# Performance work log

Measured on AMD Instinct MI355X. Metric: run time of the kernel, lower is better.

The kernel has to match this reference:

```python
import jax, jax.numpy as jnp
import numpy as np

SIZE, DIM, BATCH, K = 131072, 128, 1024, 16


def _l2_normalize(x, axis):
    return x / jnp.linalg.norm(x, axis=axis, keepdims=True)


def setup_inputs() -> dict:
    key = jax.random.key(0)
    k1, k2, k3, k4, k5 = jax.random.split(key, 5)
    # bank init as in MemoryBank._create: uniform in [-std, std], then l2-normalized rows
    std = 1.0 / np.sqrt(DIM / 3)
    bank = jax.random.uniform(k1, (SIZE, DIM), dtype=jnp.float32) * (2 * std) - std
    bank = _l2_normalize(bank, 1)
    emb_batch = _l2_normalize(jax.random.normal(k2, (BATCH, DIM), dtype=jnp.float32), 1)
    data_memory = _l2_normalize(jax.random.normal(k3, (BATCH, DIM), dtype=jnp.float32), 1)
    idxs = jax.random.randint(k4, (BATCH, K), 0, SIZE)
    update_indices = jax.random.randint(k5, (BATCH,), 0, SIZE)
    return {
        "emb_batch": emb_batch,
        "data_memory": data_memory,
        "bank": bank,
        "idxs": idxs,
        "update_indices": update_indices,
    }


def reference(emb_batch, data_memory, bank, idxs, update_indices):
    # get_all_dot_products: [B, S]
    all_dots = jnp.matmul(emb_batch, bank.T)
    # get_all_distances: ||b_j - e_i||. Original materializes [B,S,D] differences;
    # mathematically identical expansion avoids the huge intermediate.
    e_sq = jnp.sum(emb_batch * emb_batch, axis=1)[:, None]   # [B,1]
    b_sq = jnp.sum(bank * bank, axis=1)[None, :]             # [1,S]
    distances = jnp.sqrt(jnp.maximum(e_sq + b_sq - 2.0 * all_dots, 0.0))  # [B,S]
    # get_dot_products with 2D idxs: gather [B,K,D] then multiply-sum -> [B,K]
    knn_dots = jnp.einsum("bkd,bd->bk", bank[idxs], emb_batch)
    # update: scatter rows of data_memory into the bank
    new_bank = bank.at[update_indices].set(data_memory)
    return distances, all_dots, knn_dots, new_bank
```

## Files before the change

### kernel.cpp

```cpp
#include <hip/hip_runtime.h>
#include <hip/hip_bf16.h>

typedef __bf16 bf16x8 __attribute__((ext_vector_type(8)));
typedef float  f32x4  __attribute__((ext_vector_type(4)));

#define SIZE_  131072
#define DIM_   128
#define BATCH_ 1024
#define KNN_   16

#define BM 256
#define BN 64

__global__ __launch_bounds__(256) void prep_emb(const float* __restrict__ emb,
                                                __bf16* __restrict__ emb16,
                                                float* __restrict__ e_sq) {
    int wid  = (blockIdx.x * 256 + threadIdx.x) >> 6;
    int lane = threadIdx.x & 63;
    float2 v = *reinterpret_cast<const float2*>(emb + (size_t)wid * DIM_ + lane * 2);
    float s = v.x * v.x + v.y * v.y;
    #pragma unroll
    for (int off = 32; off; off >>= 1) s += __shfl_xor(s, off);
    union { __bf16 h[2]; unsigned int u; } pk;
    pk.h[0] = (__bf16)v.x; pk.h[1] = (__bf16)v.y;
    *reinterpret_cast<unsigned int*>(emb16 + (size_t)wid * DIM_ + lane * 2) = pk.u;
    if (lane == 0) e_sq[wid] = s;
}

__global__ __launch_bounds__(256) void prep_bank(const float* __restrict__ bank,
                                                 float* __restrict__ newbank,
                                                 float* __restrict__ b_sq) {
    int wid  = (blockIdx.x * 256 + threadIdx.x) >> 6;
    int lane = threadIdx.x & 63;
    size_t base = (size_t)wid * DIM_ + lane * 2;
    float2 v = *reinterpret_cast<const float2*>(bank + base);
    *reinterpret_cast<float2*>(newbank + base) = v;
    float s = v.x * v.x + v.y * v.y;
    #pragma unroll
    for (int off = 32; off; off >>= 1) s += __shfl_xor(s, off);
    if (lane == 0) b_sq[wid] = s;
}

__global__ __launch_bounds__(256) void gemm_dist(const float* __restrict__ bank,
                                                 const __bf16* __restrict__ emb16,
                                                 const float* __restrict__ e_sq,
                                                 const float* __restrict__ b_sq,
                                                 float* __restrict__ out_dist,
                                                 float* __restrict__ out_dots) {
    __shared__ __bf16 lA[BM * DIM_];
    __shared__ __bf16 lB[BN * DIM_];
    char* lAc = (char*)lA;
    char* lBc = (char*)lB;

    int bid = blockIdx.x;
    int logical = (bid & 7) * (8192 / 8) + (bid >> 3);
    int mt = logical & 3;
    int nt = logical >> 2;
    int m0 = mt * BM;
    int n0 = nt * BN;
    int tid = threadIdx.x;

    {
        const char* src = (const char*)(emb16 + (size_t)m0 * DIM_);
        #pragma unroll
        for (int i = 0; i < 16; ++i) {
            int o   = (i * 256 + tid) * 16;
            int row = o >> 8;
            int so  = o ^ ((row & 7) << 4);
            *reinterpret_cast<int4*>(lAc + so) = *reinterpret_cast<const int4*>(src + o);
        }
    }
    {
        #pragma unroll
        for (int i = 0; i < 4; ++i) {
            int p   = i * 256 + tid;
            int row = p >> 4;
            int k0  = (p & 15) * 8;
            const f32x4* s4 = reinterpret_cast<const f32x4*>(bank + (size_t)(n0 + row) * DIM_ + k0);
            f32x4 a = s4[0], b = s4[1];
            union { __bf16 h[8]; int4 v; } pk;
            pk.h[0] = (__bf16)a.x; pk.h[1] = (__bf16)a.y; pk.h[2] = (__bf16)a.z; pk.h[3] = (__bf16)a.w;
            pk.h[4] = (__bf16)b.x; pk.h[5] = (__bf16)b.y; pk.h[6] = (__bf16)b.z; pk.h[7] = (__bf16)b.w;
            int o  = (row << 8) + k0 * 2;
            int so = o ^ ((row & 7) << 4);
            *reinterpret_cast<int4*>(lBc + so) = pk.v;
        }
    }
    __syncthreads();

    int wv   = tid >> 6;
    int lane = tid & 63;
    int lr   = lane & 15;
    int lkb  = (lane >> 4) * 8;
    int rgrp = lane >> 4;

    f32x4 acc[4][4] = {};

    #pragma unroll
    for (int ks = 0; ks < 4; ++ks) {
        int kk = ks * 32 + lkb;
        bf16x8 af[4], bf[4];
        #pragma unroll
        for (int mr = 0; mr < 4; ++mr) {
            int row = wv * 64 + mr * 16 + lr;
            int o   = (row << 8) + kk * 2;
            af[mr]  = *reinterpret_cast<const bf16x8*>(lAc + (o ^ ((row & 7) << 4)));
        }
        #pragma unroll
        for (int nc = 0; nc < 4; ++nc) {
            int row = nc * 16 + lr;
            int o   = (row << 8) + kk * 2;
            bf[nc]  = *reinterpret_cast<const bf16x8*>(lBc + (o ^ ((row & 7) << 4)));
        }
        #pragma unroll
        for (int mr = 0; mr < 4; ++mr)
            #pragma unroll
            for (int nc = 0; nc < 4; ++nc)
                acc[mr][nc] = __builtin_amdgcn_mfma_f32_16x16x32_bf16(af[mr], bf[nc], acc[mr][nc], 0, 0, 0);
    }

    float bs[4];
    #pragma unroll
    for (int nc = 0; nc < 4; ++nc) bs[nc] = b_sq[n0 + nc * 16 + lr];
    float es[4][4];
    #pragma unroll
    for (int mr = 0; mr < 4; ++mr)
        #pragma unroll
        for (int j = 0; j < 4; ++j)
            es[mr][j] = e_sq[m0 + wv * 64 + mr * 16 + rgrp * 4 + j];

    __syncthreads();
    char* ftile = lAc;

    #pragma unroll
    for (int pass = 0; pass < 2; ++pass) {
        #pragma unroll
        for (int mr = 0; mr < 4; ++mr) {
            #pragma unroll
            for (int j = 0; j < 4; ++j) {
                int row = wv * 64 + mr * 16 + rgrp * 4 + j;
                #pragma unroll
                for (int nc = 0; nc < 4; ++nc) {
                    float d = acc[mr][nc][j];
                    float val;
                    if (pass == 0) {
                        float arg = es[mr][j] + bs[nc] - 2.0f * d;
                        val = sqrtf(fmaxf(arg, 0.0f));
                    } else {
                        val = d;
                    }
                    int o = (row << 8) + (nc * 16 + lr) * 4;
                    *reinterpret_cast<float*>(ftile + (o ^ ((row & 7) << 4))) = val;
                }
            }
        }
        __syncthreads();
        float* outp = pass ? out_dots : out_dist;
        int g  = tid >> 4;
        int c4 = tid & 15;
        #pragma unroll
        for (int i = 0; i < 16; ++i) {
            int row = i * 16 + g;
            int o   = (row << 8) + c4 * 16;
            f32x4 v = *reinterpret_cast<const f32x4*>(ftile + (o ^ ((row & 7) << 4)));
            size_t ga = (size_t)(m0 + row) * SIZE_ + n0 + c4 * 4;
            __builtin_nontemporal_store(v, reinterpret_cast<f32x4*>(outp + ga));
        }
        __syncthreads();
    }
}

__global__ __launch_bounds__(128) void scatter_rows(const float* __restrict__ dmem,
                                                    const int* __restrict__ upd,
                                                    float* __restrict__ newbank) {
    int i = blockIdx.x;
    int idx = upd[i];
    __shared__ int dup;
    if (threadIdx.x == 0) dup = 0;
    __syncthreads();
    for (int j = i + 1 + threadIdx.x; j < BATCH_; j += 128)
        if (upd[j] == idx) dup = 1;
    __syncthreads();
    if (dup) return;
    newbank[(size_t)idx * DIM_ + threadIdx.x] = dmem[(size_t)i * DIM_ + threadIdx.x];
}

__global__ __launch_bounds__(256) void knn_kernel(const float* __restrict__ bank,
                                                  const float* __restrict__ emb,
                                                  const int* __restrict__ idxs,
                                                  float* __restrict__ knn) {
    int wid  = (blockIdx.x * 256 + threadIdx.x) >> 6;
    int lane = threadIdx.x & 63;
    int b    = wid >> 4;
    int idx  = idxs[wid];
    float2 br = *reinterpret_cast<const float2*>(bank + (size_t)idx * DIM_ + lane * 2);
    float2 er = *reinterpret_cast<const float2*>(emb + (size_t)b * DIM_ + lane * 2);
    float s = br.x * er.x + br.y * er.y;
    #pragma unroll
    for (int off = 32; off; off >>= 1) s += __shfl_xor(s, off);
    if (lane == 0) knn[wid] = s;
}

extern "C" void kernel_launch(void* const* d_in, const int* in_sizes, int n_in,
                              void* d_out, int out_size, void* d_ws, size_t ws_size,
                              hipStream_t stream) {
    const float* emb  = (const float*)d_in[0];
    const float* dmem = (const float*)d_in[1];
    const float* bank = (const float*)d_in[2];
    const int*   idxs = (const int*)d_in[3];
    const int*   upd  = (const int*)d_in[4];

    float* out       = (float*)d_out;
    float* out_dist  = out;
    float* out_dots  = out + (size_t)BATCH_ * SIZE_;
    float* out_knn   = out + (size_t)2 * BATCH_ * SIZE_;
    float* out_bank  = out_knn + (size_t)BATCH_ * KNN_;

    char*   ws    = (char*)d_ws;
    float*  b_sq  = (float*)ws;
    float*  e_sq  = (float*)(ws + 524288);
    __bf16* emb16 = (__bf16*)(ws + 528384);

    prep_emb <<<BATCH_ / 4,      256, 0, stream>>>(emb, emb16, e_sq);
    prep_bank<<<SIZE_ / 4,       256, 0, stream>>>(bank, out_bank, b_sq);
    gemm_dist<<<(BATCH_ / BM) * (SIZE_ / BN), 256, 0, stream>>>(bank, emb16, e_sq, b_sq, out_dist, out_dots);
    scatter_rows<<<BATCH_,       128, 0, stream>>>(dmem, upd, out_bank);
    knn_kernel<<<(BATCH_ * KNN_) / 4, 256, 0, stream>>>(bank, emb, idxs, out_knn);
}
```

Before: 274.8 us.

## Fuse bank copy and squared-norm into GEMM kernel, halve M tile

Removes the separate prep_bank kernel. The GEMM blocks now compute each bank row's squared norm from the fp32 tile they already load, keep it in shared memory, and have the mt==0 blocks write the bank copy with nontemporal stores. BM drops from 256 to 128, which doubles the grid and makes each bank tile get loaded and converted 8 times instead of 4. In exchange for that extra bank read traffic, it saves one kernel launch, a full pass over the bank, and the b_sq buffer round trip.

```diff
diff --git a/kernel.cpp b/kernel.cpp
--- a/kernel.cpp
+++ b/kernel.cpp
@@ -9,8 +9,10 @@
 #define BATCH_ 1024
 #define KNN_   16
 
-#define BM 256
+#define BM 128
 #define BN 64
+#define MT (BATCH_ / BM)
+#define NT (SIZE_ / BN)
 
 __global__ __launch_bounds__(256) void prep_emb(const float* __restrict__ emb,
                                                 __bf16* __restrict__ emb16,
@@ -27,35 +29,22 @@
     if (lane == 0) e_sq[wid] = s;
 }
 
-__global__ __launch_bounds__(256) void prep_bank(const float* __restrict__ bank,
-                                                 float* __restrict__ newbank,
-                                                 float* __restrict__ b_sq) {
-    int wid  = (blockIdx.x * 256 + threadIdx.x) >> 6;
-    int lane = threadIdx.x & 63;
-    size_t base = (size_t)wid * DIM_ + lane * 2;
-    float2 v = *reinterpret_cast<const float2*>(bank + base);
-    *reinterpret_cast<float2*>(newbank + base) = v;
-    float s = v.x * v.x + v.y * v.y;
-    #pragma unroll
-    for (int off = 32; off; off >>= 1) s += __shfl_xor(s, off);
-    if (lane == 0) b_sq[wid] = s;
-}
-
 __global__ __launch_bounds__(256) void gemm_dist(const float* __restrict__ bank,
                                                  const __bf16* __restrict__ emb16,
                                                  const float* __restrict__ e_sq,
-                                                 const float* __restrict__ b_sq,
                                                  float* __restrict__ out_dist,
-                                                 float* __restrict__ out_dots) {
+                                                 float* __restrict__ out_dots,
+                                                 float* __restrict__ out_bank) {
     __shared__ __bf16 lA[BM * DIM_];
     __shared__ __bf16 lB[BN * DIM_];
+    __shared__ float  bsq[BN];
     char* lAc = (char*)lA;
     char* lBc = (char*)lB;
 
     int bid = blockIdx.x;
-    int logical = (bid & 7) * (8192 / 8) + (bid >> 3);
-    int mt = logical & 3;
-    int nt = logical >> 2;
+    int logical = (bid & 7) * (16384 / 8) + (bid >> 3);
+    int mt = logical & (MT - 1);
+    int nt = logical >> 3;
     int m0 = mt * BM;
     int n0 = nt * BN;
     int tid = threadIdx.x;
@@ -63,7 +52,7 @@
     {
         const char* src = (const char*)(emb16 + (size_t)m0 * DIM_);
         #pragma unroll
-        for (int i = 0; i < 16; ++i) {
+        for (int i = 0; i < 8; ++i) {
             int o   = (i * 256 + tid) * 16;
             int row = o >> 8;
             int so  = o ^ ((row & 7) << 4);
@@ -76,8 +65,18 @@
             int p   = i * 256 + tid;
             int row = p >> 4;
             int k0  = (p & 15) * 8;
-            const f32x4* s4 = reinterpret_cast<const f32x4*>(bank + (size_t)(n0 + row) * DIM_ + k0);
+            size_t gb = (size_t)(n0 + row) * DIM_ + k0;
+            const f32x4* s4 = reinterpret_cast<const f32x4*>(bank + gb);
             f32x4 a = s4[0], b = s4[1];
+            if (mt == 0) {
+                __builtin_nontemporal_store(a, reinterpret_cast<f32x4*>(out_bank + gb));
+                __builtin_nontemporal_store(b, reinterpret_cast<f32x4*>(out_bank + gb + 4));
+            }
+            float s = a.x * a.x + a.y * a.y + a.z * a.z + a.w * a.w
+                    + b.x * b.x + b.y * b.y + b.z * b.z + b.w * b.w;
+            #pragma unroll
+            for (int off = 8; off; off >>= 1) s += __shfl_xor(s, off);
+            if ((p & 15) == 0) bsq[row] = s;
             union { __bf16 h[8]; int4 v; } pk;
             pk.h[0] = (__bf16)a.x; pk.h[1] = (__bf16)a.y; pk.h[2] = (__bf16)a.z; pk.h[3] = (__bf16)a.w;
             pk.h[4] = (__bf16)b.x; pk.h[5] = (__bf16)b.y; pk.h[6] = (__bf16)b.z; pk.h[7] = (__bf16)b.w;
@@ -94,15 +93,15 @@
     int lkb  = (lane >> 4) * 8;
     int rgrp = lane >> 4;
 
-    f32x4 acc[4][4] = {};
+    f32x4 acc[2][4] = {};
 
     #pragma unroll
     for (int ks = 0; ks < 4; ++ks) {
         int kk = ks * 32 + lkb;
-        bf16x8 af[4], bf[4];
-        #pragma unroll
-        for (int mr = 0; mr < 4; ++mr) {
-            int row = wv * 64 + mr * 16 + lr;
+        bf16x8 af[2], bf[4];
+        #pragma unroll
+        for (int mr = 0; mr < 2; ++mr) {
+            int row = wv * 32 + mr * 16 + lr;
             int o   = (row << 8) + kk * 2;
             af[mr]  = *reinterpret_cast<const bf16x8*>(lAc + (o ^ ((row & 7) << 4)));
         }
@@ -113,7 +112,7 @@
             bf[nc]  = *reinterpret_cast<const bf16x8*>(lBc + (o ^ ((row & 7) << 4)));
         }
         #pragma unroll
-        for (int mr = 0; mr < 4; ++mr)
+        for (int mr = 0; mr < 2; ++mr)
             #pragma unroll
             for (int nc = 0; nc < 4; ++nc)
                 acc[mr][nc] = __builtin_amdgcn_mfma_f32_16x16x32_bf16(af[mr], bf[nc], acc[mr][nc], 0, 0, 0);
@@ -121,13 +120,13 @@
 
     float bs[4];
     #pragma unroll
-    for (int nc = 0; nc < 4; ++nc) bs[nc] = b_sq[n0 + nc * 16 + lr];
-    float es[4][4];
-    #pragma unroll
-    for (int mr = 0; mr < 4; ++mr)
+    for (int nc = 0; nc < 4; ++nc) bs[nc] = bsq[nc * 16 + lr];
+    float es[2][4];
+    #pragma unroll
+    for (int mr = 0; mr < 2; ++mr)
         #pragma unroll
         for (int j = 0; j < 4; ++j)
-            es[mr][j] = e_sq[m0 + wv * 64 + mr * 16 + rgrp * 4 + j];
+            es[mr][j] = e_sq[m0 + wv * 32 + mr * 16 + rgrp * 4 + j];
 
     __syncthreads();
     char* ftile = lAc;
@@ -135,10 +134,10 @@
     #pragma unroll
     for (int pass = 0; pass < 2; ++pass) {
         #pragma unroll
-        for (int mr = 0; mr < 4; ++mr) {
+        for (int mr = 0; mr < 2; ++mr) {
             #pragma unroll
             for (int j = 0; j < 4; ++j) {
-                int row = wv * 64 + mr * 16 + rgrp * 4 + j;
+                int row = wv * 32 + mr * 16 + rgrp * 4 + j;
                 #pragma unroll
                 for (int nc = 0; nc < 4; ++nc) {
                     float d = acc[mr][nc][j];
@@ -159,7 +158,7 @@
         int g  = tid >> 4;
         int c4 = tid & 15;
         #pragma unroll
-        for (int i = 0; i < 16; ++i) {
+        for (int i = 0; i < 8; ++i) {
             int row = i * 16 + g;
             int o   = (row << 8) + c4 * 16;
             f32x4 v = *reinterpret_cast<const f32x4*>(ftile + (o ^ ((row & 7) << 4)));
@@ -217,13 +216,11 @@
     float* out_bank  = out_knn + (size_t)BATCH_ * KNN_;
 
     char*   ws    = (char*)d_ws;
-    float*  b_sq  = (float*)ws;
-    float*  e_sq  = (float*)(ws + 524288);
-    __bf16* emb16 = (__bf16*)(ws + 528384);
-
-    prep_emb <<<BATCH_ / 4,      256, 0, stream>>>(emb, emb16, e_sq);
-    prep_bank<<<SIZE_ / 4,       256, 0, stream>>>(bank, out_bank, b_sq);
-    gemm_dist<<<(BATCH_ / BM) * (SIZE_ / BN), 256, 0, stream>>>(bank, emb16, e_sq, b_sq, out_dist, out_dots);
-    scatter_rows<<<BATCH_,       128, 0, stream>>>(dmem, upd, out_bank);
+    float*  e_sq  = (float*)ws;
+    __bf16* emb16 = (__bf16*)(ws + 4096);
+
+    prep_emb <<<BATCH_ / 4, 256, 0, stream>>>(emb, emb16, e_sq);
+    gemm_dist<<<MT * NT,    256, 0, stream>>>(bank, emb16, e_sq, out_dist, out_dots, out_bank);
+    scatter_rows<<<BATCH_,  128, 0, stream>>>(dmem, upd, out_bank);
     knn_kernel<<<(BATCH_ * KNN_) / 4, 256, 0, stream>>>(bank, emb, idxs, out_knn);
 }
```

Measured after the change: 261.4 us. -4.9%, faster.
